# Optimization experiments

Measured on AMD Instinct MI355X. Metric: run time of the kernel, lower is better.

Reference implementation:

```python
import jax, jax.numpy as jnp
import numpy as np

PATCH = 8
EPS_LN = 1e-5
EPS_NORM = 1e-12


def conv1x1(x, w):
    # x: [b,i,h,w], w: [o,i]
    return jnp.einsum('bihw,oi->bohw', x, w)


def dwconv3(x, w):
    # depthwise 3x3, SAME padding; w: [C,1,3,3]
    return jax.lax.conv_general_dilated(
        x, w, window_strides=(1, 1), padding='SAME',
        feature_group_count=x.shape[1],
        dimension_numbers=('NCHW', 'OIHW', 'NCHW'))


def l2norm(x, axis=-1):
    n = jnp.sqrt(jnp.sum(x * x, axis=axis, keepdims=True))
    return x / jnp.maximum(n, EPS_NORM)


def layernorm_ch(x, w, b):
    # WithBias LayerNorm over the channel dim of NCHW (matches to_3d/to_4d)
    mu = jnp.mean(x, axis=1, keepdims=True)
    var = jnp.mean((x - mu) ** 2, axis=1, keepdims=True)
    return (x - mu) / jnp.sqrt(var + EPS_LN) * w[None, :, None, None] + b[None, :, None, None]


def patchify(t, p):
    b, c, h, w = t.shape
    t = t.reshape(b, c, h // p, p, w // p, p)
    return t.transpose(0, 1, 2, 4, 3, 5)  # b c gh gw p p


def unpatchify(t):
    b, c, gh, gw, p1, p2 = t.shape
    return t.transpose(0, 1, 2, 4, 3, 5).reshape(b, c, gh * p1, gw * p2)


def setup_inputs() -> dict:
    key = jax.random.key(0)
    ks = jax.random.split(key, 12)
    b, c, h, w = 4, 128, 256, 256
    heads = 8
    s = 0.05
    inp = {
        'x': jax.random.normal(ks[0], (b, c, h, w), jnp.float32),
        'qkv_w': s * jax.random.normal(ks[1], (3 * c, c), jnp.float32),
        'qkv_dw': s * jax.random.normal(ks[2], (3 * c, 1, 3, 3), jnp.float32),
        'proj_w': s * jax.random.normal(ks[3], (c, c), jnp.float32),
        'q1_w': s * jax.random.normal(ks[4], (c, c), jnp.float32),
        'q2_w': s * jax.random.normal(ks[5], (c, c), jnp.float32),
        'kv_w': s * jax.random.normal(ks[6], (2 * c, c), jnp.float32),
        'kv_dw': s * jax.random.normal(ks[7], (2 * c, 1, 3, 3), jnp.float32),
        'projf_w': s * jax.random.normal(ks[8], (c, c), jnp.float32),
        'temperature': jnp.ones((1, heads, 1, 1), jnp.float32),
        'ln_w': jnp.ones((c,), jnp.float32),
        'ln_b': jnp.zeros((c,), jnp.float32),
    }
    return inp


def reference(x, qkv_w, qkv_dw, proj_w, q1_w, q2_w, kv_w, kv_dw, projf_w,
              temperature, ln_w, ln_b):
    b, c, h, w = x.shape
    heads = temperature.shape[1]
    ch = c // heads

    # ---- channel (transposed) attention ----
    qkv = dwconv3(conv1x1(x, qkv_w), qkv_dw)
    q, k, v = jnp.split(qkv, 3, axis=1)
    q = l2norm(q.reshape(b, heads, ch, h * w))
    k = l2norm(k.reshape(b, heads, ch, h * w))
    v = v.reshape(b, heads, ch, h * w)
    attn = jax.nn.softmax(jnp.einsum('bhcn,bhdn->bhcd', q, k) * temperature, axis=-1)
    out = conv1x1(jnp.einsum('bhcd,bhdn->bhcn', attn, v).reshape(b, c, h, w), proj_w)

    # ---- FFT gating branch ----
    x_fft = jnp.fft.fftn(x, axes=(-2, -1)).real
    x_fft3 = conv1x1(jax.nn.gelu(conv1x1(x_fft, q1_w), approximate=False), q2_w)
    qf = jnp.fft.ifftn(x_fft3, axes=(-2, -1)).real

    kvf = dwconv3(conv1x1(out, kv_w), kv_dw)
    kf, vf = jnp.split(kvf, 2, axis=1)

    qp = patchify(vf, PATCH)  # note: original names vf's patches q_patch_1
    kp = patchify(kf, PATCH)
    prod = jnp.fft.rfft2(qp) * jnp.fft.rfft2(kp)
    out_1 = jnp.fft.irfft2(prod, s=(PATCH, PATCH))
    out_1 = unpatchify(out_1)
    out_1 = layernorm_ch(out_1, ln_w, ln_b) * qf
    return conv1x1(out_1, projf_w) + out
```

## Files before the change

### kernel.cpp

```cpp
#include <hip/hip_runtime.h>
#include <math.h>

#define HW 65536
#define CPX 64
#define XSTR 136
#define RSTR 129

typedef short short8 __attribute__((ext_vector_type(8)));
typedef float f32x4 __attribute__((ext_vector_type(4)));

__device__ __forceinline__ float2 cmul(float2 a, float2 b){
  return make_float2(a.x*b.x - a.y*b.y, a.x*b.y + a.y*b.x);
}

__device__ __forceinline__ unsigned short f2bf(float f){
  unsigned u = __float_as_uint(f);
  u += 0x7fff + ((u >> 16) & 1);
  return (unsigned short)(u >> 16);
}
__device__ __forceinline__ float bf2f(unsigned short h){
  unsigned u = ((unsigned)h) << 16;
  return __uint_as_float(u);
}

__global__ __launch_bounds__(256,4) void conv1x1_mfma(
    const float* __restrict__ X, size_t bsX,
    const float* __restrict__ W, size_t bsW,
    float* __restrict__ Y, size_t bsY,
    const float* __restrict__ R, size_t bsR,
    int act)
{
  __shared__ __align__(16) unsigned short sbuf[2*CPX*XSTR];
  unsigned short* xh = sbuf;
  unsigned short* xl = sbuf + CPX*XSTR;
  const int t = threadIdx.x;
  const int l = t & 63;
  const int w = t >> 6;
  const int b = blockIdx.z;
  const int bx = ((blockIdx.x & 7) << 7) + (blockIdx.x >> 3);
  const size_t pxBase = (size_t)bx * CPX;
  const float* Xb = X + (size_t)b*bsX + pxBase;
  const float* Wb = W + (size_t)b*bsW;

  short8 whi[2][4], wlo[2][4];
  {
    const int row0 = (w<<5) + (l & 15);
    const int kg = (l >> 4) << 3;
    #pragma unroll
    for (int m=0;m<2;m++){
      #pragma unroll
      for (int ks=0;ks<4;ks++){
        const float* wp = Wb + (size_t)(row0 + 16*m)*128 + 32*ks + kg;
        float4 f0 = *(const float4*)wp;
        float4 f1 = *(const float4*)(wp+4);
        float fv[8] = {f0.x,f0.y,f0.z,f0.w,f1.x,f1.y,f1.z,f1.w};
        short8 h, lo;
        #pragma unroll
        for (int e=0;e<8;e++){
          unsigned short hb = f2bf(fv[e]);
          h[e]  = (short)hb;
          lo[e] = (short)f2bf(fv[e] - bf2f(hb));
        }
        whi[m][ks]=h; wlo[m][ks]=lo;
      }
    }
  }

  {
    const int px = (t & 15) << 2;
    const int s3 = (t & 7) << 3;
    #pragma unroll
    for (int i=0;i<8;i++){
      const int k = i*16 + (t >> 4);
      float4 v = *(const float4*)(Xb + (size_t)k*HW + px);
      const int kk = k ^ s3;
      float f[4] = {v.x,v.y,v.z,v.w};
      #pragma unroll
      for (int j=0;j<4;j++){
        unsigned short hb = f2bf(f[j]);
        xh[(px+j)*XSTR + kk] = hb;
        xl[(px+j)*XSTR + kk] = f2bf(f[j] - bf2f(hb));
      }
    }
  }
  __syncthreads();

  f32x4 acc[2][4];
  #pragma unroll
  for (int m=0;m<2;m++)
    #pragma unroll
    for (int n=0;n<4;n++) acc[m][n] = (f32x4){0.f,0.f,0.f,0.f};

  const int kg = (l>>4)<<3;
  #pragma unroll
  for (int ks=0;ks<4;ks++){
    const int k0 = 32*ks + kg;
    #pragma unroll
    for (int n=0;n<4;n++){
      const int px = 16*n + (l&15);
      const int off = px*XSTR + (k0 ^ (((px>>2)&7)<<3));
      short8 bh = *(short8*)&xh[off];
      short8 bl = *(short8*)&xl[off];
      #pragma unroll
      for (int m=0;m<2;m++){
        acc[m][n] = __builtin_amdgcn_mfma_f32_16x16x32_bf16(whi[m][ks], bh, acc[m][n], 0,0,0);
        acc[m][n] = __builtin_amdgcn_mfma_f32_16x16x32_bf16(wlo[m][ks], bh, acc[m][n], 0,0,0);
        acc[m][n] = __builtin_amdgcn_mfma_f32_16x16x32_bf16(whi[m][ks], bl, acc[m][n], 0,0,0);
      }
    }
  }
  __syncthreads();

  float* ost = (float*)sbuf;
  #pragma unroll
  for (int m=0;m<2;m++){
    const int ocb = (w<<5) + 16*m + ((l>>4)<<2);
    #pragma unroll
    for (int n=0;n<4;n++){
      const int px = 16*n + (l&15);
      #pragma unroll
      for (int r=0;r<4;r++){
        float v = acc[m][n][r];
        if (act==1) v = 0.5f*v*(1.f + erff(v*0.70710678118654752440f));
        ost[(ocb+r)*68 + px] = v;
      }
    }
  }
  __syncthreads();
  float* Yb = Y + (size_t)b*bsY + pxBase;
  const float* Rb = R ? (R + (size_t)b*bsR + pxBase) : 0;
  {
    const int px4 = (t & 15) << 2;
    #pragma unroll
    for (int it=0; it<8; it++){
      const int oc = it*16 + (t >> 4);
      float4 v4 = *(float4*)&ost[oc*68 + px4];
      if (Rb){
        float4 r4 = *(const float4*)(Rb + (size_t)oc*HW + px4);
        v4.x += r4.x; v4.y += r4.y; v4.z += r4.z; v4.w += r4.w;
      }
      *(float4*)(Yb + (size_t)oc*HW + px4) = v4;
    }
  }
}

__global__ __launch_bounds__(256,4) void conv_gate_mfma(
    const float* __restrict__ X,
    const float* __restrict__ W1, const float* __restrict__ W2,
    float* __restrict__ Y)
{
  __shared__ __align__(16) unsigned short sbuf[2*CPX*XSTR];
  unsigned short* xh = sbuf;
  unsigned short* xl = sbuf + CPX*XSTR;
  const int t = threadIdx.x;
  const int l = t & 63;
  const int w = t >> 6;
  const int b = blockIdx.z;
  const int bx = ((blockIdx.x & 7) << 7) + (blockIdx.x >> 3);
  const size_t pxBase = (size_t)bx * CPX;
  const float* Xb = X + (size_t)b*8388608 + pxBase;

  const int kg = (l>>4)<<3;
  const int row0 = (w<<5) + (l & 15);
  short8 whi[2][4], wlo[2][4];

  {
    const int px = (t & 15) << 2;
    const int s3 = (t & 7) << 3;
    #pragma unroll
    for (int i=0;i<8;i++){
      const int k = i*16 + (t >> 4);
      float4 v = *(const float4*)(Xb + (size_t)k*HW + px);
      const int kk = k ^ s3;
      float f[4] = {v.x,v.y,v.z,v.w};
      #pragma unroll
      for (int j=0;j<4;j++){
        unsigned short hb = f2bf(f[j]);
        xh[(px+j)*XSTR + kk] = hb;
        xl[(px+j)*XSTR + kk] = f2bf(f[j] - bf2f(hb));
      }
    }
  }
  #pragma unroll
  for (int m=0;m<2;m++){
    #pragma unroll
    for (int ks=0;ks<4;ks++){
      const float* wp = W1 + (size_t)(row0 + 16*m)*128 + 32*ks + kg;
      float4 f0 = *(const float4*)wp;
      float4 f1 = *(const float4*)(wp+4);
      float fv[8] = {f0.x,f0.y,f0.z,f0.w,f1.x,f1.y,f1.z,f1.w};
      short8 h, lo;
      #pragma unroll
      for (int e=0;e<8;e++){
        unsigned short hb = f2bf(fv[e]);
        h[e]  = (short)hb;
        lo[e] = (short)f2bf(fv[e] - bf2f(hb));
      }
      whi[m][ks]=h; wlo[m][ks]=lo;
    }
  }
  __syncthreads();

  f32x4 acc[2][4];
  #pragma unroll
  for (int m=0;m<2;m++)
    #pragma unroll
    for (int n=0;n<4;n++) acc[m][n] = (f32x4){0.f,0.f,0.f,0.f};
  #pragma unroll
  for (int ks=0;ks<4;ks++){
    const int k0 = 32*ks + kg;
    #pragma unroll
    for (int n=0;n<4;n++){
      const int px = 16*n + (l&15);
      const int off = px*XSTR + (k0 ^ (((px>>2)&7)<<3));
      short8 bh = *(short8*)&xh[off];
      short8 bl = *(short8*)&xl[off];
      #pragma unroll
      for (int m=0;m<2;m++){
        acc[m][n] = __builtin_amdgcn_mfma_f32_16x16x32_bf16(whi[m][ks], bh, acc[m][n], 0,0,0);
        acc[m][n] = __builtin_amdgcn_mfma_f32_16x16x32_bf16(wlo[m][ks], bh, acc[m][n], 0,0,0);
        acc[m][n] = __builtin_amdgcn_mfma_f32_16x16x32_bf16(whi[m][ks], bl, acc[m][n], 0,0,0);
      }
    }
  }
  __syncthreads();

  #pragma unroll
  for (int m=0;m<2;m++){
    const int oc0 = (w<<5) + 16*m + ((l>>4)<<2);
    #pragma unroll
    for (int n=0;n<4;n++){
      const int px = 16*n + (l&15);
      const int s3p = ((px>>2)&7)<<3;
      #pragma unroll
      for (int r=0;r<4;r++){
        float v = acc[m][n][r];
        v = 0.5f*v*(1.f + erff(v*0.70710678118654752440f));
        unsigned short hb = f2bf(v);
        const int kk = (oc0+r) ^ s3p;
        xh[px*XSTR + kk] = hb;
        xl[px*XSTR + kk] = f2bf(v - bf2f(hb));
      }
    }
  }
  #pragma unroll
  for (int m=0;m<2;m++){
    #pragma unroll
    for (int ks=0;ks<4;ks++){
      const float* wp = W2 + (size_t)(row0 + 16*m)*128 + 32*ks + kg;
      float4 f0 = *(const float4*)wp;
      float4 f1 = *(const float4*)(wp+4);
      float fv[8] = {f0.x,f0.y,f0.z,f0.w,f1.x,f1.y,f1.z,f1.w};
      short8 h, lo;
      #pragma unroll
      for (int e=0;e<8;e++){
        unsigned short hb = f2bf(fv[e]);
        h[e]  = (short)hb;
        lo[e] = (short)f2bf(fv[e] - bf2f(hb));
      }
      whi[m][ks]=h; wlo[m][ks]=lo;
    }
  }
  __syncthreads();

  #pragma unroll
  for (int m=0;m<2;m++)
    #pragma unroll
    for (int n=0;n<4;n++) acc[m][n] = (f32x4){0.f,0.f,0.f,0.f};
  #pragma unroll
  for (int ks=0;ks<4;ks++){
    const int k0 = 32*ks + kg;
    #pragma unroll
    for (int n=0;n<4;n++){
      const int px = 16*n + (l&15);
      const int off = px*XSTR + (k0 ^ (((px>>2)&7)<<3));
      short8 bh = *(short8*)&xh[off];
      short8 bl = *(short8*)&xl[off];
      #pragma unroll
      for (int m=0;m<2;m++){
        acc[m][n] = __builtin_amdgcn_mfma_f32_16x16x32_bf16(whi[m][ks], bh, acc[m][n], 0,0,0);
        acc[m][n] = __builtin_amdgcn_mfma_f32_16x16x32_bf16(wlo[m][ks], bh, acc[m][n], 0,0,0);
        acc[m][n] = __builtin_amdgcn_mfma_f32_16x16x32_bf16(whi[m][ks], bl, acc[m][n], 0,0,0);
      }
    }
  }
  __syncthreads();

  float* ost = (float*)sbuf;
  #pragma unroll
  for (int m=0;m<2;m++){
    const int ocb = (w<<5) + 16*m + ((l>>4)<<2);
    #pragma unroll
    for (int n=0;n<4;n++){
      const int px = 16*n + (l&15);
      #pragma unroll
      for (int r=0;r<4;r++) ost[(ocb+r)*68 + px] = acc[m][n][r];
    }
  }
  __syncthreads();
  float* Yb = Y + (size_t)b*8388608 + pxBase;
  {
    const int px4 = (t & 15) << 2;
    #pragma unroll
    for (int it=0; it<8; it++){
      const int oc = it*16 + (t >> 4);
      float4 v4 = *(float4*)&ost[oc*68 + px4];
      *(float4*)(Yb + (size_t)oc*HW + px4) = v4;
    }
  }
}

template<int NOUT>
__global__ __launch_bounds__(256,3) void convN_mfma(
    const float* __restrict__ X, size_t bsX,
    const float* __restrict__ W,
    float* __restrict__ Y, size_t bsY, size_t ostep)
{
  __shared__ __align__(16) unsigned short sbuf[2*CPX*XSTR];
  __shared__ __align__(16) float tbuf[64*68];
  unsigned short* xh = sbuf;
  unsigned short* xl = sbuf + CPX*XSTR;
  const int t = threadIdx.x;
  const int l = t & 63;
  const int w = t >> 6;
  const int b = blockIdx.z;
  const int bx = ((blockIdx.x & 7) << 7) + (blockIdx.x >> 3);
  const size_t pxBase = (size_t)bx * CPX;
  const float* Xb = X + (size_t)b*bsX + pxBase;

  {
    const int px = (t & 15) << 2;
    const int s3 = (t & 7) << 3;
    #pragma unroll
    for (int i=0;i<8;i++){
      const int k = i*16 + (t >> 4);
      float4 v = *(const float4*)(Xb + (size_t)k*HW + px);
      const int kk = k ^ s3;
      float f[4] = {v.x,v.y,v.z,v.w};
      #pragma unroll
      for (int j=0;j<4;j++){
        unsigned short hb = f2bf(f[j]);
        xh[(px+j)*XSTR + kk] = hb;
        xl[(px+j)*XSTR + kk] = f2bf(f[j] - bf2f(hb));
      }
    }
  }
  __syncthreads();

  const int kg = (l>>4)<<3;
  const int row0 = (w<<5) + (l & 15);

  #pragma unroll
  for (int o=0; o<NOUT; ++o){
    short8 whi[2][4], wlo[2][4];
    {
      const float* Wo = W + (size_t)o*16384;
      #pragma unroll
      for (int m=0;m<2;m++){
        #pragma unroll
        for (int ks=0;ks<4;ks++){
          const float* wp = Wo + (size_t)(row0 + 16*m)*128 + 32*ks + kg;
          float4 f0 = *(const float4*)wp;
          float4 f1 = *(const float4*)(wp+4);
          float fv[8] = {f0.x,f0.y,f0.z,f0.w,f1.x,f1.y,f1.z,f1.w};
          short8 h, lo;
          #pragma unroll
          for (int e=0;e<8;e++){
            unsigned short hb = f2bf(fv[e]);
            h[e]  = (short)hb;
            lo[e] = (short)f2bf(fv[e] - bf2f(hb));
          }
          whi[m][ks]=h; wlo[m][ks]=lo;
        }
      }
    }
    f32x4 acc[2][4];
    #pragma unroll
    for (int m=0;m<2;m++)
      #pragma unroll
      for (int n=0;n<4;n++) acc[m][n] = (f32x4){0.f,0.f,0.f,0.f};
    #pragma unroll
    for (int ks=0;ks<4;ks++){
      const int k0 = 32*ks + kg;
      #pragma unroll
      for (int n=0;n<4;n++){
        const int px = 16*n + (l&15);
        const int off = px*XSTR + (k0 ^ (((px>>2)&7)<<3));
        short8 bh = *(short8*)&xh[off];
        short8 bl = *(short8*)&xl[off];
        #pragma unroll
        for (int m=0;m<2;m++){
          acc[m][n] = __builtin_amdgcn_mfma_f32_16x16x32_bf16(whi[m][ks], bh, acc[m][n], 0,0,0);
          acc[m][n] = __builtin_amdgcn_mfma_f32_16x16x32_bf16(wlo[m][ks], bh, acc[m][n], 0,0,0);
          acc[m][n] = __builtin_amdgcn_mfma_f32_16x16x32_bf16(whi[m][ks], bl, acc[m][n], 0,0,0);
        }
      }
    }
    float* Yb = Y + (size_t)o*ostep + (size_t)b*bsY + pxBase;
    #pragma unroll
    for (int half=0; half<2; ++half){
      __syncthreads();
      if ((w >> 1) == half){
        #pragma unroll
        for (int m=0;m<2;m++){
          const int ocl = ((w&1)<<5) + 16*m + ((l>>4)<<2);
          #pragma unroll
          for (int n=0;n<4;n++){
            const int px = 16*n + (l&15);
            #pragma unroll
            for (int r=0;r<4;r++) tbuf[(ocl+r)*68 + px] = acc[m][n][r];
          }
        }
      }
      __syncthreads();
      {
        const int px4 = (t & 15) << 2;
        #pragma unroll
        for (int it=0; it<4; it++){
          const int ocl = it*16 + (t >> 4);
          float4 v4 = *(float4*)&tbuf[ocl*68 + px4];
          *(float4*)(Yb + (size_t)(64*half + ocl)*HW + px4) = v4;
        }
      }
    }
    __syncthreads();
  }
}

__global__ __launch_bounds__(256,4) void dwconv3_row_k(
    const float* __restrict__ in, const float* __restrict__ w9,
    float* __restrict__ out, float* __restrict__ sqpart, int chOff)
{
  __shared__ float tl[34][256];
  int z = blockIdx.x;
  int cch = z & 127;
  int y0 = blockIdx.y * 32;
  size_t base = (size_t)z * HW;
  int t = threadIdx.x;
  float wv[9];
  #pragma unroll
  for (int i=0;i<9;i++) wv[i] = w9[cch*9+i];
  for (int idx = t; idx < 34*64; idx += 256){
    int r = idx >> 6, c4 = (idx & 63) << 2;
    int gy = y0 + r - 1;
    float4 v = make_float4(0.f,0.f,0.f,0.f);
    if ((unsigned)gy < 256u) v = *(const float4*)(in + base + (size_t)gy*256 + c4);
    *(float4*)&tl[r][c4] = v;
  }
  __syncthreads();
  const int ct = t;
  float ss = 0.f;
  for (int r = 0; r < 32; ++r){
    float acc = 0.f;
    #pragma unroll
    for (int dy=0; dy<3; dy++){
      float a  = (ct>0)   ? tl[r+dy][ct-1] : 0.f;
      float bm = tl[r+dy][ct];
      float c2 = (ct<255) ? tl[r+dy][ct+1] : 0.f;
      acc = fmaf(wv[dy*3+0], a, fmaf(wv[dy*3+1], bm, fmaf(wv[dy*3+2], c2, acc)));
    }
    out[base + (size_t)(y0+r)*256 + ct] = acc;
    ss += acc*acc;
  }
  if (sqpart){
    #pragma unroll
    for (int o=32;o>0;o>>=1) ss += __shfl_down(ss, o);
    __shared__ float red[4];
    if ((t&63)==0) red[t>>6] = ss;
    __syncthreads();
    if (t==0){
      float s = red[0]+red[1]+red[2]+red[3];
      int pg = ((z>>7)<<8) + chOff + cch;
      sqpart[pg*8 + blockIdx.y] = s;
    }
  }
}

__global__ __launch_bounds__(256) void qk_gram_k(
    const float* __restrict__ q, const float* __restrict__ k, float* __restrict__ Gp)
{
  __shared__ float qs[16][65], ks[16][65];
  int s = blockIdx.x, h = blockIdx.y, b = blockIdx.z;
  int t = threadIdx.x;
  int c = t >> 4, d = t & 15;
  const float* qb = q + ((size_t)b*128 + h*16)*HW + (size_t)s*1024;
  const float* kb = k + ((size_t)b*128 + h*16)*HW + (size_t)s*1024;
  float acc = 0.f;
  for (int n0=0;n0<1024;n0+=64){
    #pragma unroll
    for (int it=0;it<4;it++){
      int idx = it*256 + t;
      int row = idx >> 6, col = idx & 63;
      qs[row][col] = qb[(size_t)row*HW + n0 + col];
      ks[row][col] = kb[(size_t)row*HW + n0 + col];
    }
    __syncthreads();
    #pragma unroll
    for (int nn=0;nn<64;nn++) acc = fmaf(qs[c][nn], ks[d][nn], acc);
    __syncthreads();
  }
  Gp[(((size_t)b*8 + h)*64 + s)*256 + t] = acc;
}

__global__ __launch_bounds__(256) void attn_weff_k(
    const float* __restrict__ Gp, const float* __restrict__ sqpart,
    const float* __restrict__ temp, const float* __restrict__ proj_w,
    float* __restrict__ Weff)
{
  int b = blockIdx.x, t = threadIdx.x;
  __shared__ float G[8][16][16];
  __shared__ float A[8][16][16];
  __shared__ float rn_s[256];
  {
    const float* pp = sqpart + ((size_t)b*256 + t)*8;
    float s = 0.f;
    #pragma unroll
    for (int i=0;i<8;i++) s += pp[i];
    rn_s[t] = 1.f/fmaxf(sqrtf(s), 1e-12f);
  }
  __syncthreads();
  for (int e = t; e < 2048; e += 256){
    int h = e >> 8, cd = e & 255;
    int c = cd >> 4, d = cd & 15;
    const float* gp = Gp + (((size_t)b*8 + h)*64)*256 + cd;
    float sum = 0.f;
    for (int s2=0;s2<64;s2++) sum += gp[(size_t)s2*256];
    G[h][c][d] = sum * rn_s[h*16 + c] * rn_s[128 + h*16 + d] * temp[h];
  }
  __syncthreads();
  if (t < 128){
    int h = t >> 4, c = t & 15;
    float m = -1e30f;
    for (int d=0;d<16;d++) m = fmaxf(m, G[h][c][d]);
    float e[16], ssum = 0.f;
    for (int d=0;d<16;d++){ e[d] = expf(G[h][c][d]-m); ssum += e[d]; }
    float inv = 1.f/ssum;
    for (int d=0;d<16;d++) A[h][c][d] = e[d]*inv;
  }
  __syncthreads();
  for (int idx = t; idx < 16384; idx += 256){
    int o = idx >> 7, hd = idx & 127;
    int h = hd >> 4, d = hd & 15;
    float acc = 0.f;
    #pragma unroll
    for (int c=0;c<16;c++) acc = fmaf(proj_w[o*128 + h*16 + c], A[h][c][d], acc);
    Weff[((size_t)b*128 + o)*128 + hd] = acc;
  }
}

__global__ __launch_bounds__(256) void patch_circ_k(
    const float* __restrict__ vf, const float* __restrict__ kf, float* __restrict__ out)
{
  __shared__ float vs[32*68];
  __shared__ float ks2[32*68];
  size_t base = (size_t)blockIdx.y*HW + (size_t)blockIdx.x*2048;
  int t = threadIdx.x;
  #pragma unroll
  for (int it=0; it<2; it++){
    int idx = it*256 + t;
    int row = idx >> 6;
    int c4  = (idx & 63) << 2;
    float4 v  = *(const float4*)(vf + base + (size_t)row*256 + c4);
    float4 kv = *(const float4*)(kf + base + (size_t)row*256 + c4);
    int p = c4 >> 3, j0 = c4 & 7;
    *(float4*)&vs [p*68 + row*8 + j0] = v;
    *(float4*)&ks2[p*68 + row*8 + j0] = kv;
  }
  __syncthreads();
  int p = t & 31, pr = t >> 5;
  float acc[8];
  #pragma unroll
  for (int q=0;q<8;q++) acc[q]=0.f;
  #pragma unroll
  for (int i=0;i<8;i++){
    float4 va = *(float4*)&vs[p*68 + i*8];
    float4 vb = *(float4*)&vs[p*68 + i*8 + 4];
    int kr = (pr - i) & 7;
    float4 ka = *(float4*)&ks2[p*68 + kr*8];
    float4 kb = *(float4*)&ks2[p*68 + kr*8 + 4];
    float vv[8]={va.x,va.y,va.z,va.w,vb.x,vb.y,vb.z,vb.w};
    float kk[8]={ka.x,ka.y,ka.z,ka.w,kb.x,kb.y,kb.z,kb.w};
    #pragma unroll
    for (int q=0;q<8;q++)
      #pragma unroll
      for (int j=0;j<8;j++)
        acc[q] = fmaf(vv[j], kk[(q-j)&7], acc[q]);
  }
  float* op = out + base + (size_t)pr*256 + p*8;
  *(float4*)op     = make_float4(acc[0],acc[1],acc[2],acc[3]);
  *(float4*)(op+4) = make_float4(acc[4],acc[5],acc[6],acc[7]);
}

__global__ __launch_bounds__(64) void fft256_rows2_r2c_half(
    const float* __restrict__ in, size_t inStride,
    float2* __restrict__ out, size_t outStride, float dir)
{
  __shared__ float2 buf[2][256];
  __shared__ float2 tw[128];
  int t = threadIdx.x;
  size_t rp = blockIdx.x;
  const float* ipa = in + (size_t)blockIdx.y*inStride + rp*512;
  const float* ipb = ipa + 256;
  float2* opa = out + (size_t)blockIdx.y*outStride + rp*2*RSTR;
  float2* opb = opa + RSTR;
  for (int i = t; i < 128; i += 64){
    float ang = 6.283185307179586477f * (float)i / 256.f;
    float s, c;
    sincosf(ang, &s, &c);
    tw[i] = make_float2(c, dir*s);
  }
  for (int i=t;i<256;i+=64) buf[0][i] = make_float2(ipa[i], ipb[i]);
  int cur = 0, m = 1;
  for (int st=0; st<8; st++){
    __syncthreads();
    #pragma unroll
    for (int p2=0;p2<2;p2++){
      int bf = t + (p2<<6);
      int k = bf & (m-1);
      int jm = bf - k;
      float2 a = buf[cur][k + jm];
      float2 c = buf[cur][k + jm + 128];
      float2 w = tw[jm];
      float2 sm = make_float2(a.x+c.x, a.y+c.y);
      float2 df = make_float2(a.x-c.x, a.y-c.y);
      buf[cur^1][k + 2*jm]     = sm;
      buf[cur^1][k + 2*jm + m] = cmul(w, df);
    }
    cur ^= 1; m <<= 1;
  }
  __syncthreads();
  for (int u=t; u<=128; u+=64){
    float2 z = buf[cur][u];
    float2 mm = buf[cur][(256-u)&255];
    opa[u] = make_float2(0.5f*(z.x+mm.x), 0.5f*(z.y-mm.y));
    opb[u] = make_float2(0.5f*(z.y+mm.y), 0.5f*(mm.x-z.x));
  }
}

__global__ __launch_bounds__(256,4) void fft256_cols_c2r_herm(
    const float2* __restrict__ in, size_t inStride,
    float* __restrict__ out, size_t outStride,
    float dir, float scale)
{
  __shared__ float2 buf[16*257];
  __shared__ float2 tw[128];
  const int t = threadIdx.x;
  const int col = t & 15, rr = t >> 4;
  const int u0 = blockIdx.x << 4;
  const int u  = u0 + col;
  const int plane = blockIdx.y;
  const bool valid = (u <= 128);
  const float2* ip = in + (size_t)blockIdx.z*inStride + (size_t)plane*(256*RSTR) + u;
  if (t < 128){
    float ang = 6.283185307179586477f * (float)t / 256.f;
    float s, c;
    sincosf(ang, &s, &c);
    tw[t] = make_float2(c, dir*s);
  }
  #pragma unroll
  for (int i=0;i<16;i++){
    int r = i*16 + rr;
    float2 v = valid ? ip[(size_t)r*RSTR] : make_float2(0.f,0.f);
    int br = __brev((unsigned)r) >> 24;
    buf[col*257 + br] = v;
  }
  __syncthreads();
  for (int s=1;s<=8;s++){
    const int half = 1 << (s-1);
    const int tsh = 8 - s;
    #pragma unroll
    for (int j=0;j<8;j++){
      int bfi = rr + (j<<4);
      int lo = bfi & (half-1);
      int p  = ((bfi >> (s-1)) << s) + lo;
      float2 uq = buf[col*257 + p];
      float2 vq = buf[col*257 + p + half];
      float2 w  = tw[lo << tsh];
      float2 wv = cmul(w, vq);
      buf[col*257 + p]        = make_float2(uq.x+wv.x, uq.y+wv.y);
      buf[col*257 + p + half] = make_float2(uq.x-wv.x, uq.y-wv.y);
    }
    __syncthreads();
  }
  float* op = out + (size_t)blockIdx.z*outStride + (size_t)plane*HW;
  if (u0 < 128){
    const int c0 = (t & 3) << 2;
    #pragma unroll
    for (int i=0;i<4;i++){
      int r = i*64 + (t >> 2);
      float4 o4 = make_float4(buf[(c0+0)*257 + r].x * scale,
                              buf[(c0+1)*257 + r].x * scale,
                              buf[(c0+2)*257 + r].x * scale,
                              buf[(c0+3)*257 + r].x * scale);
      *(float4*)(op + (size_t)r*256 + u0 + c0) = o4;
    }
    const int um = u0 + col;
    if (um >= 1 && um <= 127){
      const int mc = 256 - um;
      #pragma unroll
      for (int i=0;i<16;i++){
        int r2 = i*16 + rr;
        int src = (256 - r2) & 255;
        op[(size_t)r2*256 + mc] = buf[col*257 + src].x * scale;
      }
    }
  } else {
    int r2 = t;
    op[(size_t)r2*256 + 128] = buf[0*257 + r2].x * scale;
  }
}

__global__ __launch_bounds__(256) void ln_mul_k(
    const float* __restrict__ x, const float* __restrict__ qf,
    const float* __restrict__ lw, const float* __restrict__ lb,
    float* __restrict__ y)
{
  int b = blockIdx.y;
  size_t px0 = (size_t)blockIdx.x*64;
  int t = threadIdx.x;
  int px = t & 63, g = t >> 6;
  const float* xp = x + (size_t)b*8388608 + px0 + px;
  float vals[32];
  float s1 = 0.f, s2 = 0.f;
  #pragma unroll
  for (int i=0;i<32;i++){
    float v = xp[(size_t)(g*32+i)*HW];
    vals[i] = v; s1 += v; s2 += v*v;
  }
  __shared__ float r1[4][64], r2[4][64];
  r1[g][px] = s1; r2[g][px] = s2;
  __syncthreads();
  float S1 = r1[0][px]+r1[1][px]+r1[2][px]+r1[3][px];
  float S2 = r2[0][px]+r2[1][px]+r2[2][px]+r2[3][px];
  float mu = S1 * (1.f/128.f);
  float var = S2 * (1.f/128.f) - mu*mu;
  float rstd = rsqrtf(var + 1e-5f);
  const float* qp = qf + (size_t)b*8388608 + px0 + px;
  float* yp = y + (size_t)b*8388608 + px0 + px;
  #pragma unroll
  for (int i=0;i<32;i++){
    int c = g*32 + i;
    float v = (vals[i]-mu)*rstd*lw[c] + lb[c];
    yp[(size_t)c*HW] = v * qp[(size_t)c*HW];
  }
}

extern "C" void kernel_launch(void* const* d_in, const int* in_sizes, int n_in,
                              void* d_out, int out_size, void* d_ws, size_t ws_size,
                              hipStream_t stream)
{
  const float* x       = (const float*)d_in[0];
  const float* qkv_w   = (const float*)d_in[1];
  const float* qkv_dw  = (const float*)d_in[2];
  const float* proj_w  = (const float*)d_in[3];
  const float* q1_w    = (const float*)d_in[4];
  const float* q2_w    = (const float*)d_in[5];
  const float* kv_w    = (const float*)d_in[6];
  const float* kv_dw   = (const float*)d_in[7];
  const float* projf_w = (const float*)d_in[8];
  const float* temp    = (const float*)d_in[9];
  const float* ln_w    = (const float*)d_in[10];
  const float* ln_b    = (const float*)d_in[11];
  float* out = (float*)d_out;
  float* ws  = (float*)d_ws;

  const size_t P  = 33554432;
  const size_t CB = 8388608;
  const size_t HSTR = 32768u*RSTR;
  float* A = ws;
  float* B = ws + P;
  float* C = ws + 2*P;
  float* sqpart = ws + 3*P;
  float* Gp     = sqpart + 8192;
  float* Weff   = Gp + 524288;

  dim3 cg(1024,1,4); dim3 cb(256);
  dim3 dg(512,8);  dim3 db(256);

  convN_mfma<3><<<cg,cb,0,stream>>>(x, CB, qkv_w, A, CB, P);
  dwconv3_row_k<<<dg,db,0,stream>>>(A, qkv_dw + 0*1152, out, sqpart, 0);
  dwconv3_row_k<<<dg,db,0,stream>>>(B, qkv_dw + 1*1152, A, sqpart, 128);
  qk_gram_k<<<dim3(64,8,4),256,0,stream>>>(out, A, Gp);
  attn_weff_k<<<4,256,0,stream>>>(Gp, sqpart, temp, proj_w, Weff);
  dwconv3_row_k<<<dg,db,0,stream>>>(C, qkv_dw + 2*1152, B, nullptr, 0);
  conv1x1_mfma<<<cg,cb,0,stream>>>(B, CB, Weff, 16384, C, CB, nullptr, 0, 0);
  convN_mfma<2><<<cg,cb,0,stream>>>(C, CB, kv_w, A, CB, P);
  dwconv3_row_k<<<dg,db,0,stream>>>(A, kv_dw + 0*1152, out, nullptr, 0);
  dwconv3_row_k<<<dg,db,0,stream>>>(B, kv_dw + 1*1152, A, nullptr, 0);
  patch_circ_k<<<dim3(32,512),256,0,stream>>>(A, out, B);
  for (int b=0;b<4;b+=2){
    fft256_rows2_r2c_half<<<dim3(16384,2),64,0,stream>>>(x + (size_t)b*CB, CB, (float2*)A, HSTR, -1.f);
    fft256_cols_c2r_herm<<<dim3(9,128,2),256,0,stream>>>((const float2*)A, HSTR, out + (size_t)b*CB, CB, -1.f, 1.f);
  }
  conv_gate_mfma<<<cg,cb,0,stream>>>(out, q1_w, q2_w, out);
  for (int b=0;b<4;b+=2){
    fft256_rows2_r2c_half<<<dim3(16384,2),64,0,stream>>>(out + (size_t)b*CB, CB, (float2*)A, HSTR, 1.f);
    fft256_cols_c2r_herm<<<dim3(9,128,2),256,0,stream>>>((const float2*)A, HSTR, out + (size_t)b*CB, CB, 1.f, 1.f/65536.f);
  }
  ln_mul_k<<<dim3(1024,4),256,0,stream>>>(B, out, ln_w, ln_b, A);
  conv1x1_mfma<<<cg,cb,0,stream>>>(A, CB, projf_w, 0, out, CB, C, CB, 0);
}
```

Baseline: 1.523 ms.

## Fold kv_w into attention weights and fuse kv depthwise conv into patch kernel

```diff
diff --git a/kernel.cpp b/kernel.cpp
--- a/kernel.cpp
+++ b/kernel.cpp
@@ -313,7 +313,7 @@
 template<int NOUT>
 __global__ __launch_bounds__(256,3) void convN_mfma(
     const float* __restrict__ X, size_t bsX,
-    const float* __restrict__ W,
+    const float* __restrict__ W, size_t bsW,
     float* __restrict__ Y, size_t bsY, size_t ostep)
 {
   __shared__ __align__(16) unsigned short sbuf[2*CPX*XSTR];
@@ -327,6 +327,7 @@
   const int bx = ((blockIdx.x & 7) << 7) + (blockIdx.x >> 3);
   const size_t pxBase = (size_t)bx * CPX;
   const float* Xb = X + (size_t)b*bsX + pxBase;
+  const float* Wbase = W + (size_t)b*bsW;
 
   {
     const int px = (t & 15) << 2;
@@ -354,7 +355,7 @@
   for (int o=0; o<NOUT; ++o){
     short8 whi[2][4], wlo[2][4];
     {
-      const float* Wo = W + (size_t)o*16384;
+      const float* Wo = Wbase + (size_t)o*16384;
       #pragma unroll
       for (int m=0;m<2;m++){
         #pragma unroll
@@ -427,6 +428,37 @@
   }
 }
 
+__global__ __launch_bounds__(256) void wcomb_k(
+    const float* __restrict__ kv_w, float* __restrict__ Wcomb)
+{
+  int m = blockIdx.x, b = blockIdx.y;
+  const float* We = Wcomb + (size_t)b*49152;
+  float* Wo = Wcomb + (size_t)b*49152 + (size_t)(m+1)*16384;
+  const float* kw = kv_w + (size_t)m*16384;
+  int t = threadIdx.x;
+  int o = t & 127, half = t >> 7;
+  const int d0 = half*64;
+  float acc[64];
+  #pragma unroll
+  for (int i=0;i<64;i++) acc[i]=0.f;
+  for (int c=0;c<128;c++){
+    float kv = kw[o*128 + c];
+    const float* wr = We + c*128 + d0;
+    #pragma unroll
+    for (int i=0;i<64;i+=4){
+      float4 w4 = *(const float4*)(wr + i);
+      acc[i]   = fmaf(kv, w4.x, acc[i]);
+      acc[i+1] = fmaf(kv, w4.y, acc[i+1]);
+      acc[i+2] = fmaf(kv, w4.z, acc[i+2]);
+      acc[i+3] = fmaf(kv, w4.w, acc[i+3]);
+    }
+  }
+  float* wo = Wo + o*128 + d0;
+  #pragma unroll
+  for (int i=0;i<64;i+=4)
+    *(float4*)(wo+i) = make_float4(acc[i],acc[i+1],acc[i+2],acc[i+3]);
+}
+
 __global__ __launch_bounds__(256,4) void dwconv3_row_k(
     const float* __restrict__ in, const float* __restrict__ w9,
     float* __restrict__ out, float* __restrict__ sqpart, int chOff)
@@ -505,7 +537,7 @@
 __global__ __launch_bounds__(256) void attn_weff_k(
     const float* __restrict__ Gp, const float* __restrict__ sqpart,
     const float* __restrict__ temp, const float* __restrict__ proj_w,
-    float* __restrict__ Weff)
+    float* __restrict__ Wcomb)
 {
   int b = blockIdx.x, t = threadIdx.x;
   __shared__ float G[8][16][16];
@@ -544,27 +576,56 @@
     float acc = 0.f;
     #pragma unroll
     for (int c=0;c<16;c++) acc = fmaf(proj_w[o*128 + h*16 + c], A[h][c][d], acc);
-    Weff[((size_t)b*128 + o)*128 + hd] = acc;
-  }
-}
-
-__global__ __launch_bounds__(256) void patch_circ_k(
-    const float* __restrict__ vf, const float* __restrict__ kf, float* __restrict__ out)
-{
+    Wcomb[(size_t)b*49152 + idx] = acc;
+  }
+}
+
+__global__ __launch_bounds__(256,4) void patch_dw_circ_k(
+    const float* __restrict__ kfr, const float* __restrict__ vfr,
+    const float* __restrict__ dw, float* __restrict__ out)
+{
+  __shared__ float kraw[10*256];
+  __shared__ float vraw[10*256];
   __shared__ float vs[32*68];
   __shared__ float ks2[32*68];
-  size_t base = (size_t)blockIdx.y*HW + (size_t)blockIdx.x*2048;
+  int z = blockIdx.y;
+  int cch = z & 127;
+  int y0 = blockIdx.x * 8;
+  size_t base = (size_t)z * HW;
   int t = threadIdx.x;
-  #pragma unroll
-  for (int it=0; it<2; it++){
-    int idx = it*256 + t;
-    int row = idx >> 6;
-    int c4  = (idx & 63) << 2;
-    float4 v  = *(const float4*)(vf + base + (size_t)row*256 + c4);
-    float4 kv = *(const float4*)(kf + base + (size_t)row*256 + c4);
-    int p = c4 >> 3, j0 = c4 & 7;
-    *(float4*)&vs [p*68 + row*8 + j0] = v;
-    *(float4*)&ks2[p*68 + row*8 + j0] = kv;
+  float wk[9], wv2[9];
+  #pragma unroll
+  for (int i=0;i<9;i++){ wk[i] = dw[cch*9+i]; wv2[i] = dw[(128+cch)*9+i]; }
+  for (int idx = t; idx < 10*64; idx += 256){
+    int r = idx >> 6, c4 = (idx & 63) << 2;
+    int gy = y0 + r - 1;
+    float4 kv = make_float4(0.f,0.f,0.f,0.f), vv = kv;
+    if ((unsigned)gy < 256u){
+      kv = *(const float4*)(kfr + base + (size_t)gy*256 + c4);
+      vv = *(const float4*)(vfr + base + (size_t)gy*256 + c4);
+    }
+    *(float4*)&kraw[r*256 + c4] = kv;
+    *(float4*)&vraw[r*256 + c4] = vv;
+  }
+  __syncthreads();
+  const int ct = t;
+  const int pp = ct >> 3, jj = ct & 7;
+  #pragma unroll
+  for (int r=0;r<8;r++){
+    float ak = 0.f, av = 0.f;
+    #pragma unroll
+    for (int dy=0;dy<3;dy++){
+      float kl = (ct>0)   ? kraw[(r+dy)*256+ct-1] : 0.f;
+      float km = kraw[(r+dy)*256+ct];
+      float kr2= (ct<255) ? kraw[(r+dy)*256+ct+1] : 0.f;
+      ak = fmaf(wk[dy*3+0],kl, fmaf(wk[dy*3+1],km, fmaf(wk[dy*3+2],kr2, ak)));
+      float vl = (ct>0)   ? vraw[(r+dy)*256+ct-1] : 0.f;
+      float vm = vraw[(r+dy)*256+ct];
+      float vr2= (ct<255) ? vraw[(r+dy)*256+ct+1] : 0.f;
+      av = fmaf(wv2[dy*3+0],vl, fmaf(wv2[dy*3+1],vm, fmaf(wv2[dy*3+2],vr2, av)));
+    }
+    ks2[pp*68 + r*8 + jj] = ak;
+    vs [pp*68 + r*8 + jj] = av;
   }
   __syncthreads();
   int p = t & 31, pr = t >> 5;
@@ -586,7 +647,7 @@
       for (int j=0;j<8;j++)
         acc[q] = fmaf(vv[j], kk[(q-j)&7], acc[q]);
   }
-  float* op = out + base + (size_t)pr*256 + p*8;
+  float* op = out + base + (size_t)(y0+pr)*256 + p*8;
   *(float4*)op     = make_float4(acc[0],acc[1],acc[2],acc[3]);
   *(float4*)(op+4) = make_float4(acc[4],acc[5],acc[6],acc[7]);
 }
@@ -772,31 +833,29 @@
   float* C = ws + 2*P;
   float* sqpart = ws + 3*P;
   float* Gp     = sqpart + 8192;
-  float* Weff   = Gp + 524288;
+  float* Wcomb  = Gp + 524288;
 
   dim3 cg(1024,1,4); dim3 cb(256);
   dim3 dg(512,8);  dim3 db(256);
 
-  convN_mfma<3><<<cg,cb,0,stream>>>(x, CB, qkv_w, A, CB, P);
+  convN_mfma<3><<<cg,cb,0,stream>>>(x, CB, qkv_w, 0, A, CB, P);
   dwconv3_row_k<<<dg,db,0,stream>>>(A, qkv_dw + 0*1152, out, sqpart, 0);
   dwconv3_row_k<<<dg,db,0,stream>>>(B, qkv_dw + 1*1152, A, sqpart, 128);
   qk_gram_k<<<dim3(64,8,4),256,0,stream>>>(out, A, Gp);
-  attn_weff_k<<<4,256,0,stream>>>(Gp, sqpart, temp, proj_w, Weff);
+  attn_weff_k<<<4,256,0,stream>>>(Gp, sqpart, temp, proj_w, Wcomb);
+  wcomb_k<<<dim3(2,4),256,0,stream>>>(kv_w, Wcomb);
   dwconv3_row_k<<<dg,db,0,stream>>>(C, qkv_dw + 2*1152, B, nullptr, 0);
-  conv1x1_mfma<<<cg,cb,0,stream>>>(B, CB, Weff, 16384, C, CB, nullptr, 0, 0);
-  convN_mfma<2><<<cg,cb,0,stream>>>(C, CB, kv_w, A, CB, P);
-  dwconv3_row_k<<<dg,db,0,stream>>>(A, kv_dw + 0*1152, out, nullptr, 0);
-  dwconv3_row_k<<<dg,db,0,stream>>>(B, kv_dw + 1*1152, A, nullptr, 0);
-  patch_circ_k<<<dim3(32,512),256,0,stream>>>(A, out, B);
+  convN_mfma<3><<<cg,cb,0,stream>>>(B, CB, Wcomb, 49152, A, CB, P);
+  patch_dw_circ_k<<<dim3(32,512),256,0,stream>>>(B, C, kv_dw, out);
   for (int b=0;b<4;b+=2){
-    fft256_rows2_r2c_half<<<dim3(16384,2),64,0,stream>>>(x + (size_t)b*CB, CB, (float2*)A, HSTR, -1.f);
-    fft256_cols_c2r_herm<<<dim3(9,128,2),256,0,stream>>>((const float2*)A, HSTR, out + (size_t)b*CB, CB, -1.f, 1.f);
-  }
-  conv_gate_mfma<<<cg,cb,0,stream>>>(out, q1_w, q2_w, out);
+    fft256_rows2_r2c_half<<<dim3(16384,2),64,0,stream>>>(x + (size_t)b*CB, CB, (float2*)B, HSTR, -1.f);
+    fft256_cols_c2r_herm<<<dim3(9,128,2),256,0,stream>>>((const float2*)B, HSTR, C + (size_t)b*CB, CB, -1.f, 1.f);
+  }
+  conv_gate_mfma<<<cg,cb,0,stream>>>(C, q1_w, q2_w, C);
   for (int b=0;b<4;b+=2){
-    fft256_rows2_r2c_half<<<dim3(16384,2),64,0,stream>>>(out + (size_t)b*CB, CB, (float2*)A, HSTR, 1.f);
-    fft256_cols_c2r_herm<<<dim3(9,128,2),256,0,stream>>>((const float2*)A, HSTR, out + (size_t)b*CB, CB, 1.f, 1.f/65536.f);
-  }
-  ln_mul_k<<<dim3(1024,4),256,0,stream>>>(B, out, ln_w, ln_b, A);
-  conv1x1_mfma<<<cg,cb,0,stream>>>(A, CB, projf_w, 0, out, CB, C, CB, 0);
-}
+    fft256_rows2_r2c_half<<<dim3(16384,2),64,0,stream>>>(C + (size_t)b*CB, CB, (float2*)B, HSTR, 1.f);
+    fft256_cols_c2r_herm<<<dim3(9,128,2),256,0,stream>>>((const float2*)B, HSTR, C + (size_t)b*CB, CB, 1.f, 1.f/65536.f);
+  }
+  ln_mul_k<<<dim3(1024,4),256,0,stream>>>(out, C, ln_w, ln_b, B);
+  conv1x1_mfma<<<cg,cb,0,stream>>>(B, CB, projf_w, 0, out, CB, A, CB, 0);
+}
```

Result: no change. 1.534 ms (+0.7%).

## Fold kv projection into attention output weights and fuse into one 3-way conv

Applied to the files above, without the earlier changes.

```diff
diff --git a/kernel.cpp b/kernel.cpp
--- a/kernel.cpp
+++ b/kernel.cpp
@@ -313,7 +313,7 @@
 template<int NOUT>
 __global__ __launch_bounds__(256,3) void convN_mfma(
     const float* __restrict__ X, size_t bsX,
-    const float* __restrict__ W,
+    const float* __restrict__ W, size_t bsW,
     float* __restrict__ Y, size_t bsY, size_t ostep)
 {
   __shared__ __align__(16) unsigned short sbuf[2*CPX*XSTR];
@@ -327,6 +327,7 @@
   const int bx = ((blockIdx.x & 7) << 7) + (blockIdx.x >> 3);
   const size_t pxBase = (size_t)bx * CPX;
   const float* Xb = X + (size_t)b*bsX + pxBase;
+  const float* Wbase = W + (size_t)b*bsW;
 
   {
     const int px = (t & 15) << 2;
@@ -354,7 +355,7 @@
   for (int o=0; o<NOUT; ++o){
     short8 whi[2][4], wlo[2][4];
     {
-      const float* Wo = W + (size_t)o*16384;
+      const float* Wo = Wbase + (size_t)o*16384;
       #pragma unroll
       for (int m=0;m<2;m++){
         #pragma unroll
@@ -427,6 +428,37 @@
   }
 }
 
+__global__ __launch_bounds__(256) void wcomb_k(
+    const float* __restrict__ kv_w, float* __restrict__ Wcomb)
+{
+  int m = blockIdx.x, b = blockIdx.y;
+  const float* We = Wcomb + (size_t)b*49152;
+  float* Wo = Wcomb + (size_t)b*49152 + (size_t)(m+1)*16384;
+  const float* kw = kv_w + (size_t)m*16384;
+  int t = threadIdx.x;
+  int o = t & 127, half = t >> 7;
+  const int d0 = half*64;
+  float acc[64];
+  #pragma unroll
+  for (int i=0;i<64;i++) acc[i]=0.f;
+  for (int c=0;c<128;c++){
+    float kv = kw[o*128 + c];
+    const float* wr = We + c*128 + d0;
+    #pragma unroll
+    for (int i=0;i<64;i+=4){
+      float4 w4 = *(const float4*)(wr + i);
+      acc[i]   = fmaf(kv, w4.x, acc[i]);
+      acc[i+1] = fmaf(kv, w4.y, acc[i+1]);
+      acc[i+2] = fmaf(kv, w4.z, acc[i+2]);
+      acc[i+3] = fmaf(kv, w4.w, acc[i+3]);
+    }
+  }
+  float* wo = Wo + o*128 + d0;
+  #pragma unroll
+  for (int i=0;i<64;i+=4)
+    *(float4*)(wo+i) = make_float4(acc[i],acc[i+1],acc[i+2],acc[i+3]);
+}
+
 __global__ __launch_bounds__(256,4) void dwconv3_row_k(
     const float* __restrict__ in, const float* __restrict__ w9,
     float* __restrict__ out, float* __restrict__ sqpart, int chOff)
@@ -505,7 +537,7 @@
 __global__ __launch_bounds__(256) void attn_weff_k(
     const float* __restrict__ Gp, const float* __restrict__ sqpart,
     const float* __restrict__ temp, const float* __restrict__ proj_w,
-    float* __restrict__ Weff)
+    float* __restrict__ Wcomb)
 {
   int b = blockIdx.x, t = threadIdx.x;
   __shared__ float G[8][16][16];
@@ -544,7 +576,7 @@
     float acc = 0.f;
     #pragma unroll
     for (int c=0;c<16;c++) acc = fmaf(proj_w[o*128 + h*16 + c], A[h][c][d], acc);
-    Weff[((size_t)b*128 + o)*128 + hd] = acc;
+    Wcomb[(size_t)b*49152 + idx] = acc;
   }
 }
 
@@ -772,31 +804,31 @@
   float* C = ws + 2*P;
   float* sqpart = ws + 3*P;
   float* Gp     = sqpart + 8192;
-  float* Weff   = Gp + 524288;
+  float* Wcomb  = Gp + 524288;
 
   dim3 cg(1024,1,4); dim3 cb(256);
   dim3 dg(512,8);  dim3 db(256);
 
-  convN_mfma<3><<<cg,cb,0,stream>>>(x, CB, qkv_w, A, CB, P);
+  convN_mfma<3><<<cg,cb,0,stream>>>(x, CB, qkv_w, 0, A, CB, P);
   dwconv3_row_k<<<dg,db,0,stream>>>(A, qkv_dw + 0*1152, out, sqpart, 0);
   dwconv3_row_k<<<dg,db,0,stream>>>(B, qkv_dw + 1*1152, A, sqpart, 128);
   qk_gram_k<<<dim3(64,8,4),256,0,stream>>>(out, A, Gp);
-  attn_weff_k<<<4,256,0,stream>>>(Gp, sqpart, temp, proj_w, Weff);
+  attn_weff_k<<<4,256,0,stream>>>(Gp, sqpart, temp, proj_w, Wcomb);
+  wcomb_k<<<dim3(2,4),256,0,stream>>>(kv_w, Wcomb);
   dwconv3_row_k<<<dg,db,0,stream>>>(C, qkv_dw + 2*1152, B, nullptr, 0);
-  conv1x1_mfma<<<cg,cb,0,stream>>>(B, CB, Weff, 16384, C, CB, nullptr, 0, 0);
-  convN_mfma<2><<<cg,cb,0,stream>>>(C, CB, kv_w, A, CB, P);
-  dwconv3_row_k<<<dg,db,0,stream>>>(A, kv_dw + 0*1152, out, nullptr, 0);
-  dwconv3_row_k<<<dg,db,0,stream>>>(B, kv_dw + 1*1152, A, nullptr, 0);
-  patch_circ_k<<<dim3(32,512),256,0,stream>>>(A, out, B);
+  convN_mfma<3><<<cg,cb,0,stream>>>(B, CB, Wcomb, 49152, A, CB, P);
+  dwconv3_row_k<<<dg,db,0,stream>>>(B, kv_dw + 0*1152, out, nullptr, 0);
+  dwconv3_row_k<<<dg,db,0,stream>>>(C, kv_dw + 1*1152, B, nullptr, 0);
+  patch_circ_k<<<dim3(32,512),256,0,stream>>>(B, out, C);
   for (int b=0;b<4;b+=2){
-    fft256_rows2_r2c_half<<<dim3(16384,2),64,0,stream>>>(x + (size_t)b*CB, CB, (float2*)A, HSTR, -1.f);
-    fft256_cols_c2r_herm<<<dim3(9,128,2),256,0,stream>>>((const float2*)A, HSTR, out + (size_t)b*CB, CB, -1.f, 1.f);
+    fft256_rows2_r2c_half<<<dim3(16384,2),64,0,stream>>>(x + (size_t)b*CB, CB, (float2*)B, HSTR, -1.f);
+    fft256_cols_c2r_herm<<<dim3(9,128,2),256,0,stream>>>((const float2*)B, HSTR, out + (size_t)b*CB, CB, -1.f, 1.f);
   }
   conv_gate_mfma<<<cg,cb,0,stream>>>(out, q1_w, q2_w, out);
   for (int b=0;b<4;b+=2){
-    fft256_rows2_r2c_half<<<dim3(16384,2),64,0,stream>>>(out + (size_t)b*CB, CB, (float2*)A, HSTR, 1.f);
-    fft256_cols_c2r_herm<<<dim3(9,128,2),256,0,stream>>>((const float2*)A, HSTR, out + (size_t)b*CB, CB, 1.f, 1.f/65536.f);
-  }
-  ln_mul_k<<<dim3(1024,4),256,0,stream>>>(B, out, ln_w, ln_b, A);
-  conv1x1_mfma<<<cg,cb,0,stream>>>(A, CB, projf_w, 0, out, CB, C, CB, 0);
-}
+    fft256_rows2_r2c_half<<<dim3(16384,2),64,0,stream>>>(out + (size_t)b*CB, CB, (float2*)B, HSTR, 1.f);
+    fft256_cols_c2r_herm<<<dim3(9,128,2),256,0,stream>>>((const float2*)B, HSTR, out + (size_t)b*CB, CB, 1.f, 1.f/65536.f);
+  }
+  ln_mul_k<<<dim3(1024,4),256,0,stream>>>(C, out, ln_w, ln_b, B);
+  conv1x1_mfma<<<cg,cb,0,stream>>>(B, CB, projf_w, 0, out, CB, A, CB, 0);
+}
```

Measured after the change: 1.608 ms. 1.06x slower.
